# Kernel optimization log

Measured on AMD Instinct MI355X. Metric: run time of the kernel, lower is better.

The kernel has to match this reference:

```python
import jax, jax.numpy as jnp
import numpy as np

N_QUBITS = 10
N_LAYERS = 4


def setup_inputs() -> dict:
    key = jax.random.key(0)
    k1, k2 = jax.random.split(key)
    x = jax.random.normal(k1, (4, 1024, 64), dtype=jnp.float32)
    params = jax.random.normal(k2, (N_LAYERS, N_QUBITS), dtype=jnp.float32)
    return {"x": x, "params": params}


def _apply_ry(state, q, theta):
    # state: [N] + [2]*n (wire 0 is the most-significant axis, PennyLane convention)
    # theta: scalar (shared angle) or [N] (per-sample angle)
    theta = jnp.asarray(theta)
    c = jnp.cos(theta * 0.5)
    s = jnp.sin(theta * 0.5)
    if theta.ndim == 1:  # per-sample angle -> broadcast over the qubit axes
        shp = (-1,) + (1,) * (state.ndim - 2)
        c = c.reshape(shp)
        s = s.reshape(shp)
    s0 = jax.lax.index_in_dim(state, 0, axis=q + 1, keepdims=False)
    s1 = jax.lax.index_in_dim(state, 1, axis=q + 1, keepdims=False)
    # RY = [[cos, -sin], [sin, cos]] (real matrix -> state stays real)
    return jnp.stack([c * s0 - s * s1, s * s0 + c * s1], axis=q + 1)


def _apply_cnot(state, ctrl, tgt):
    a0 = jax.lax.index_in_dim(state, 0, axis=ctrl + 1, keepdims=False)
    a1 = jax.lax.index_in_dim(state, 1, axis=ctrl + 1, keepdims=False)
    # after removing the control axis, axes beyond it shift down by one
    t_axis = tgt + 1 if tgt < ctrl else tgt
    a1 = jnp.flip(a1, axis=t_axis)  # X on target within the control=1 slab
    return jnp.stack([a0, a1], axis=ctrl + 1)


def reference(x, params):
    B, T, H = x.shape
    L, n = params.shape
    N = B * T
    xf = x.reshape(N, H)[:, :n]  # encoding angles, [N, n]
    # initial |0...0> statevector, batched over all B*T tokens
    state = jnp.zeros((N, 2 ** n), dtype=x.dtype).at[:, 0].set(1.0)
    state = state.reshape((N,) + (2,) * n)
    for l in range(L):
        for q in range(n):
            state = _apply_ry(state, q, params[l, q])
        for q in range(n - 1):
            state = _apply_cnot(state, q, q + 1)
        state = _apply_cnot(state, n - 1, 0)
    for q in range(n):
        state = _apply_ry(state, q, xf[:, q])
    probs = state * state  # real amplitudes -> |amp|^2
    z = []
    for q in range(n):
        axes = tuple(a for a in range(1, n + 1) if a != q + 1)
        p = probs.sum(axis=axes)  # [N, 2]
        z.append(p[:, 0] - p[:, 1])  # <Z_q> = P(0) - P(1)
    out = jnp.stack(z, axis=-1).reshape(B, T, n)
    if H > n:
        out = jnp.concatenate([out, jnp.zeros((B, T, H - n), dtype=out.dtype)], axis=-1)
    return out
```

## Files before the change

kernel.cpp:

```cpp
#include <hip/hip_runtime.h>
#include <math.h>

#define NQ 10
#define NL 4

__global__ __launch_bounds__(256) void qc_fused(const float* __restrict__ x,
                                                const float* __restrict__ params,
                                                float* __restrict__ out) {
    __shared__ float csc[NL * NQ];
    __shared__ float css[NL * NQ];
    __shared__ __align__(16) float bufA[1024];
    __shared__ __align__(16) float bufB[1024];
    __shared__ __align__(16) float red[20][260];
    __shared__ float red2[20][4];
    __shared__ float sAB[20];

    const int tid  = threadIdx.x;
    const int w    = tid >> 6;
    const int lane = tid & 63;

    const int i  = blockIdx.x * 256 + tid;
    const int h0 = (i << 2) & 63;
    const bool act = (h0 < 12);
    float c0 = 0, s0 = 0, c1 = 0, s1 = 0, c2 = 0, s2 = 0, c3 = 0, s3 = 0;
    if (act) {
        const float4 xv = reinterpret_cast<const float4*>(x)[i];
        __sincosf(xv.x, &s0, &c0);
        __sincosf(xv.y, &s1, &c1);
        if (h0 + 2 < NQ) {
            __sincosf(xv.z, &s2, &c2);
            __sincosf(xv.w, &s3, &c3);
        }
    }

    if (tid < NL * NQ) {
        float sv, cv;
        __sincosf(0.5f * params[tid], &sv, &cv);
        csc[tid] = cv;
        css[tid] = sv;
    }

    int src[4];
#pragma unroll
    for (int r = 0; r < 4; ++r) {
        int t = (tid << 2) | r;
        t ^= (t & 1) << 9;
#pragma unroll
        for (int j = 8; j >= 0; --j)
            t ^= ((t >> (9 - j)) & 1) << (8 - j);
        src[r] = t;
    }

    float v[4] = {0.f, 0.f, 0.f, 0.f};
    if (tid == 0) v[0] = 1.0f;

    float4* bufA4 = reinterpret_cast<float4*>(bufA);
    float4* bufB4 = reinterpret_cast<float4*>(bufB);

#pragma unroll
    for (int l = 0; l < NL; ++l) {
        bufA4[tid] = make_float4(v[0], v[1], v[2], v[3]);
        __syncthreads();
        {
            const float cq0 = csc[l * NQ + 0], sq0 = css[l * NQ + 0];
            const float cq1 = csc[l * NQ + 1], sq1 = css[l * NQ + 1];
            const int a = w >> 1, b = w & 1;
            float m[4];
#pragma unroll
            for (int wp = 0; wp < 4; ++wp) {
                const int ap = wp >> 1, bp = wp & 1;
                const float e0 = (a == ap) ? cq0 : ((ap > a) ? -sq0 : sq0);
                const float e1 = (b == bp) ? cq1 : ((bp > b) ? -sq1 : sq1);
                m[wp] = e0 * e1;
            }
            const float4 u0 = bufA4[lane];
            const float4 u1 = bufA4[64 + lane];
            const float4 u2 = bufA4[128 + lane];
            const float4 u3 = bufA4[192 + lane];
            v[0] = m[0] * u0.x + m[1] * u1.x + m[2] * u2.x + m[3] * u3.x;
            v[1] = m[0] * u0.y + m[1] * u1.y + m[2] * u2.y + m[3] * u3.y;
            v[2] = m[0] * u0.z + m[1] * u1.z + m[2] * u2.z + m[3] * u3.z;
            v[3] = m[0] * u0.w + m[1] * u1.w + m[2] * u2.w + m[3] * u3.w;
        }
#pragma unroll
        for (int q = 2; q < 8; ++q) {
            const float c = csc[l * NQ + q], s = css[l * NQ + q];
            const int bit = 1 << (7 - q);
            const float t = (lane & bit) ? s : -s;
#pragma unroll
            for (int r = 0; r < 4; ++r) {
                const float p = __shfl_xor(v[r], bit, 64);
                v[r] = fmaf(t, p, c * v[r]);
            }
        }
        {
            const float c8 = csc[l * NQ + 8], s8 = css[l * NQ + 8];
            const float n0 = fmaf(-s8, v[2], c8 * v[0]);
            const float n2 = fmaf( s8, v[0], c8 * v[2]);
            const float n1 = fmaf(-s8, v[3], c8 * v[1]);
            const float n3 = fmaf( s8, v[1], c8 * v[3]);
            const float c9 = csc[l * NQ + 9], s9 = css[l * NQ + 9];
            v[0] = fmaf(-s9, n1, c9 * n0);
            v[1] = fmaf( s9, n0, c9 * n1);
            v[2] = fmaf(-s9, n3, c9 * n2);
            v[3] = fmaf( s9, n2, c9 * n3);
        }
        bufB4[tid] = make_float4(v[0], v[1], v[2], v[3]);
        __syncthreads();
#pragma unroll
        for (int r = 0; r < 4; ++r) v[r] = bufB[src[r]];
    }

    bufA4[tid] = make_float4(v[0], v[1], v[2], v[3]);
    __syncthreads();
    const float4 p0 = bufA4[((w ^ 2) << 6) | lane];
    const float4 p1 = bufA4[((w ^ 1) << 6) | lane];

    const float E = v[0] * v[0] + v[1] * v[1] + v[2] * v[2] + v[3] * v[3];
    float pA[NQ], pB[NQ];
    pA[0] = (w & 2) ? -E : E;
    pA[1] = (w & 1) ? -E : E;
    pB[0] = v[0] * p0.x + v[1] * p0.y + v[2] * p0.z + v[3] * p0.w;
    pB[1] = v[0] * p1.x + v[1] * p1.y + v[2] * p1.z + v[3] * p1.w;
#pragma unroll
    for (int q = 2; q < 8; ++q) {
        const int bit = 1 << (7 - q);
        pA[q] = (lane & bit) ? -E : E;
        float b = 0.0f;
#pragma unroll
        for (int r = 0; r < 4; ++r)
            b = fmaf(v[r], __shfl_xor(v[r], bit, 64), b);
        pB[q] = b;
    }
    pA[8] = v[0] * v[0] + v[1] * v[1] - v[2] * v[2] - v[3] * v[3];
    pB[8] = 2.0f * (v[0] * v[2] + v[1] * v[3]);
    pA[9] = v[0] * v[0] - v[1] * v[1] + v[2] * v[2] - v[3] * v[3];
    pB[9] = 2.0f * (v[0] * v[1] + v[2] * v[3]);

#pragma unroll
    for (int q = 0; q < NQ; ++q) {
        red[q][tid]      = pA[q];
        red[10 + q][tid] = pB[q];
    }
    __syncthreads();
    if (tid < 80) {
        const int q = tid >> 2, seg = tid & 3;
        const float4* row = reinterpret_cast<const float4*>(&red[q][seg * 64]);
        float4 a = row[0];
#pragma unroll
        for (int j = 1; j < 16; ++j) {
            const float4 t = row[j];
            a.x += t.x; a.y += t.y; a.z += t.z; a.w += t.w;
        }
        red2[q][seg] = (a.x + a.y) + (a.z + a.w);
    }
    __syncthreads();
    if (tid < 20)
        sAB[tid] = (red2[tid][0] + red2[tid][1]) + (red2[tid][2] + red2[tid][3]);
    __syncthreads();

    float4 o = make_float4(0.f, 0.f, 0.f, 0.f);
    if (act) {
        o.x = c0 * sAB[h0]     - s0 * sAB[10 + h0];
        o.y = c1 * sAB[h0 + 1] - s1 * sAB[10 + h0 + 1];
        if (h0 + 2 < NQ) {
            o.z = c2 * sAB[h0 + 2] - s2 * sAB[10 + h0 + 2];
            o.w = c3 * sAB[h0 + 3] - s3 * sAB[10 + h0 + 3];
        }
    }
    reinterpret_cast<float4*>(out)[i] = o;
}

extern "C" void kernel_launch(void* const* d_in, const int* in_sizes, int n_in,
                              void* d_out, int out_size, void* d_ws, size_t ws_size,
                              hipStream_t stream) {
    const float* x      = (const float*)d_in[0];
    const float* params = (const float*)d_in[1];
    float* out = (float*)d_out;

    const int total4 = out_size / 4;
    qc_fused<<<total4 / 256, 256, 0, stream>>>(x, params, out);
}
```

Baseline: 58.70 us.

## Skip first-layer simulation via product state and fold CNOT permutation into reads

Computes the first layer's RY output analytically as a product state, since the initial state is |0...0>, instead of simulating it. The CNOT-ring permutation is folded into the shared-memory read indices of the next stage, which removes one sync and buffer round trip per layer. Pairs of shuffle-based RY gates are fused into one 2-qubit update, the trig tables are cached in registers, and the final reduction uses multiple accumulators. In exchange there are more scattered LDS reads, possible bank conflicts, and more register pressure.

```diff
diff --git a/kernel.cpp b/kernel.cpp
--- a/kernel.cpp
+++ b/kernel.cpp
@@ -3,6 +3,13 @@
 
 #define NQ 10
 #define NL 4
+
+__host__ __device__ constexpr int csigma(int t) {
+    t ^= (t & 1) << 9;
+    for (int j = 8; j >= 0; --j)
+        t ^= ((t >> (9 - j)) & 1) << (8 - j);
+    return t;
+}
 
 __global__ __launch_bounds__(256) void qc_fused(const float* __restrict__ x,
                                                 const float* __restrict__ params,
@@ -39,98 +46,115 @@
         csc[tid] = cv;
         css[tid] = sv;
     }
-
-    int src[4];
-#pragma unroll
-    for (int r = 0; r < 4; ++r) {
-        int t = (tid << 2) | r;
-        t ^= (t & 1) << 9;
-#pragma unroll
-        for (int j = 8; j >= 0; --j)
-            t ^= ((t >> (9 - j)) & 1) << (8 - j);
-        src[r] = t;
-    }
-
-    float v[4] = {0.f, 0.f, 0.f, 0.f};
-    if (tid == 0) v[0] = 1.0f;
-
-    float4* bufA4 = reinterpret_cast<float4*>(bufA);
-    float4* bufB4 = reinterpret_cast<float4*>(bufB);
-
-#pragma unroll
-    for (int l = 0; l < NL; ++l) {
-        bufA4[tid] = make_float4(v[0], v[1], v[2], v[3]);
-        __syncthreads();
+    __syncthreads();
+
+    float C[NL * NQ], S[NL * NQ];
+#pragma unroll
+    for (int j = 0; j < NL * NQ / 4; ++j) {
+        reinterpret_cast<float4*>(C)[j] = reinterpret_cast<const float4*>(csc)[j];
+        reinterpret_cast<float4*>(S)[j] = reinterpret_cast<const float4*>(css)[j];
+    }
+
+    float v[4];
+    {
+        float p = 1.0f;
+#pragma unroll
+        for (int q = 0; q < 8; ++q)
+            p *= ((tid >> (7 - q)) & 1) ? S[q] : C[q];
+        const float p8c = p * C[8], p8s = p * S[8];
+        v[0] = p8c * C[9]; v[1] = p8c * S[9];
+        v[2] = p8s * C[9]; v[3] = p8s * S[9];
+    }
+    reinterpret_cast<float4*>(bufA)[tid] = make_float4(v[0], v[1], v[2], v[3]);
+    __syncthreads();
+
+    const int sig_lane = csigma(lane << 2);
+
+#pragma unroll
+    for (int l = 1; l < NL; ++l) {
+        const float* src = (l & 1) ? bufA : bufB;
+        float* dst = (l & 1) ? bufB : bufA;
+
+        const float cq0 = C[l * NQ + 0], sq0 = S[l * NQ + 0];
+        const float cq1 = C[l * NQ + 1], sq1 = S[l * NQ + 1];
+        const int a = w >> 1, b = w & 1;
+        float m[4];
+#pragma unroll
+        for (int wp = 0; wp < 4; ++wp) {
+            const int ap = wp >> 1, bp = wp & 1;
+            const float e0 = (a == ap) ? cq0 : ((ap > a) ? -sq0 : sq0);
+            const float e1 = (b == bp) ? cq1 : ((bp > b) ? -sq1 : sq1);
+            m[wp] = e0 * e1;
+        }
+        float u[4][4];
+#pragma unroll
+        for (int wp = 0; wp < 4; ++wp)
+#pragma unroll
+            for (int r = 0; r < 4; ++r)
+                u[wp][r] = src[sig_lane ^ csigma((wp << 8) | r)];
+#pragma unroll
+        for (int r = 0; r < 4; ++r)
+            v[r] = fmaf(m[3], u[3][r], fmaf(m[2], u[2][r],
+                   fmaf(m[1], u[1][r], m[0] * u[0][r])));
+
+#pragma unroll
+        for (int pr = 0; pr < 3; ++pr) {
+            const int qa = 2 + 2 * pr, qb = qa + 1;
+            const int ma = 1 << (7 - qa), mb = 1 << (7 - qb);
+            const float ca = C[l * NQ + qa], sa = S[l * NQ + qa];
+            const float cb = C[l * NQ + qb], sb = S[l * NQ + qb];
+            const float ea = (lane & ma) ? sa : -sa;
+            const float eb = (lane & mb) ? sb : -sb;
+            const float kaa = ca * cb, kab = ca * eb, kba = ea * cb, kbb = ea * eb;
+#pragma unroll
+            for (int r = 0; r < 4; ++r) {
+                const float pa  = __shfl_xor(v[r], ma, 64);
+                const float pb  = __shfl_xor(v[r], mb, 64);
+                const float pab = __shfl_xor(v[r], ma | mb, 64);
+                v[r] = fmaf(kbb, pab, fmaf(kba, pa, fmaf(kab, pb, kaa * v[r])));
+            }
+        }
+
         {
-            const float cq0 = csc[l * NQ + 0], sq0 = css[l * NQ + 0];
-            const float cq1 = csc[l * NQ + 1], sq1 = css[l * NQ + 1];
-            const int a = w >> 1, b = w & 1;
-            float m[4];
-#pragma unroll
-            for (int wp = 0; wp < 4; ++wp) {
-                const int ap = wp >> 1, bp = wp & 1;
-                const float e0 = (a == ap) ? cq0 : ((ap > a) ? -sq0 : sq0);
-                const float e1 = (b == bp) ? cq1 : ((bp > b) ? -sq1 : sq1);
-                m[wp] = e0 * e1;
-            }
-            const float4 u0 = bufA4[lane];
-            const float4 u1 = bufA4[64 + lane];
-            const float4 u2 = bufA4[128 + lane];
-            const float4 u3 = bufA4[192 + lane];
-            v[0] = m[0] * u0.x + m[1] * u1.x + m[2] * u2.x + m[3] * u3.x;
-            v[1] = m[0] * u0.y + m[1] * u1.y + m[2] * u2.y + m[3] * u3.y;
-            v[2] = m[0] * u0.z + m[1] * u1.z + m[2] * u2.z + m[3] * u3.z;
-            v[3] = m[0] * u0.w + m[1] * u1.w + m[2] * u2.w + m[3] * u3.w;
-        }
-#pragma unroll
-        for (int q = 2; q < 8; ++q) {
-            const float c = csc[l * NQ + q], s = css[l * NQ + q];
-            const int bit = 1 << (7 - q);
-            const float t = (lane & bit) ? s : -s;
-#pragma unroll
-            for (int r = 0; r < 4; ++r) {
-                const float p = __shfl_xor(v[r], bit, 64);
-                v[r] = fmaf(t, p, c * v[r]);
-            }
-        }
-        {
-            const float c8 = csc[l * NQ + 8], s8 = css[l * NQ + 8];
+            const float c8 = C[l * NQ + 8], s8 = S[l * NQ + 8];
             const float n0 = fmaf(-s8, v[2], c8 * v[0]);
             const float n2 = fmaf( s8, v[0], c8 * v[2]);
             const float n1 = fmaf(-s8, v[3], c8 * v[1]);
             const float n3 = fmaf( s8, v[1], c8 * v[3]);
-            const float c9 = csc[l * NQ + 9], s9 = css[l * NQ + 9];
+            const float c9 = C[l * NQ + 9], s9 = S[l * NQ + 9];
             v[0] = fmaf(-s9, n1, c9 * n0);
             v[1] = fmaf( s9, n0, c9 * n1);
             v[2] = fmaf(-s9, n3, c9 * n2);
             v[3] = fmaf( s9, n2, c9 * n3);
         }
-        bufB4[tid] = make_float4(v[0], v[1], v[2], v[3]);
+        reinterpret_cast<float4*>(dst)[tid] = make_float4(v[0], v[1], v[2], v[3]);
         __syncthreads();
-#pragma unroll
-        for (int r = 0; r < 4; ++r) v[r] = bufB[src[r]];
-    }
-
-    bufA4[tid] = make_float4(v[0], v[1], v[2], v[3]);
-    __syncthreads();
-    const float4 p0 = bufA4[((w ^ 2) << 6) | lane];
-    const float4 p1 = bufA4[((w ^ 1) << 6) | lane];
+    }
+
+    const int sig_tid = sig_lane ^ csigma(w << 8);
+    float p0[4], p1[4];
+#pragma unroll
+    for (int r = 0; r < 4; ++r) {
+        v[r]  = bufB[sig_tid ^ csigma(r)];
+        p0[r] = bufB[sig_tid ^ csigma(512 | r)];
+        p1[r] = bufB[sig_tid ^ csigma(256 | r)];
+    }
 
     const float E = v[0] * v[0] + v[1] * v[1] + v[2] * v[2] + v[3] * v[3];
     float pA[NQ], pB[NQ];
     pA[0] = (w & 2) ? -E : E;
     pA[1] = (w & 1) ? -E : E;
-    pB[0] = v[0] * p0.x + v[1] * p0.y + v[2] * p0.z + v[3] * p0.w;
-    pB[1] = v[0] * p1.x + v[1] * p1.y + v[2] * p1.z + v[3] * p1.w;
+    pB[0] = v[0] * p0[0] + v[1] * p0[1] + v[2] * p0[2] + v[3] * p0[3];
+    pB[1] = v[0] * p1[0] + v[1] * p1[1] + v[2] * p1[2] + v[3] * p1[3];
 #pragma unroll
     for (int q = 2; q < 8; ++q) {
         const int bit = 1 << (7 - q);
         pA[q] = (lane & bit) ? -E : E;
-        float b = 0.0f;
+        float bsum = 0.0f;
 #pragma unroll
         for (int r = 0; r < 4; ++r)
-            b = fmaf(v[r], __shfl_xor(v[r], bit, 64), b);
-        pB[q] = b;
+            bsum = fmaf(v[r], __shfl_xor(v[r], bit, 64), bsum);
+        pB[q] = bsum;
     }
     pA[8] = v[0] * v[0] + v[1] * v[1] - v[2] * v[2] - v[3] * v[3];
     pB[8] = 2.0f * (v[0] * v[2] + v[1] * v[3]);
@@ -146,13 +170,18 @@
     if (tid < 80) {
         const int q = tid >> 2, seg = tid & 3;
         const float4* row = reinterpret_cast<const float4*>(&red[q][seg * 64]);
-        float4 a = row[0];
-#pragma unroll
-        for (int j = 1; j < 16; ++j) {
-            const float4 t = row[j];
-            a.x += t.x; a.y += t.y; a.z += t.z; a.w += t.w;
-        }
-        red2[q][seg] = (a.x + a.y) + (a.z + a.w);
+        float4 a0 = row[0], a1 = row[1], a2 = row[2], a3 = row[3];
+#pragma unroll
+        for (int j = 4; j < 16; j += 4) {
+            const float4 t0 = row[j], t1 = row[j + 1], t2 = row[j + 2], t3 = row[j + 3];
+            a0.x += t0.x; a0.y += t0.y; a0.z += t0.z; a0.w += t0.w;
+            a1.x += t1.x; a1.y += t1.y; a1.z += t1.z; a1.w += t1.w;
+            a2.x += t2.x; a2.y += t2.y; a2.z += t2.z; a2.w += t2.w;
+            a3.x += t3.x; a3.y += t3.y; a3.z += t3.z; a3.w += t3.w;
+        }
+        a0.x += a1.x; a0.y += a1.y; a0.z += a1.z; a0.w += a1.w;
+        a2.x += a3.x; a2.y += a3.y; a2.z += a3.z; a2.w += a3.w;
+        red2[q][seg] = (a0.x + a0.y) + (a0.z + a0.w) + (a2.x + a2.y) + (a2.z + a2.w);
     }
     __syncthreads();
     if (tid < 20)
```

Result: faster. 57.35 us (-2.3%).
